# Kernel optimization log

Hardware: AMD Instinct MI355X
Metric: run time of the kernel (lower is better)

Reference implementation:

```python
import jax, jax.numpy as jnp
import numpy as np

KH, KW, PAD = 7, 7, 3  # 7x7 window, 'same' padding, stride 1


def setup_inputs() -> dict:
    key = jax.random.key(0)
    ks = jax.random.split(key, 7)
    b, c, h, w = 4, 256, 32, 32
    fc = 256
    rel_size = fc // 2
    ws = 1.0 / np.sqrt(c)
    rb = 1.0 / np.sqrt(rel_size)
    x = jax.random.normal(ks[0], (b, c, h, w), dtype=jnp.float32)
    Wq = jax.random.normal(ks[1], (c, fc), dtype=jnp.float32) * ws
    Wk = jax.random.normal(ks[2], (c, fc), dtype=jnp.float32) * ws
    Wv = jax.random.normal(ks[3], (c, fc), dtype=jnp.float32) * ws
    rel_x = jax.random.uniform(ks[4], (KW, rel_size), minval=-rb, maxval=rb, dtype=jnp.float32)
    rel_y = jax.random.uniform(ks[5], (KH, fc - rel_size), minval=-rb, maxval=rb, dtype=jnp.float32)
    bias = jax.random.uniform(ks[6], (fc,), minval=-1.0 / np.sqrt(fc), maxval=1.0 / np.sqrt(fc), dtype=jnp.float32)
    return {"x": x, "Wq": Wq, "Wk": Wk, "Wv": Wv, "rel_x": rel_x, "rel_y": rel_y, "bias": bias}


def _windows(t, kh, kw, pad):
    # t: (b, f, h, w) -> (b, f, kh*kw, h, w); stride-1 'same' window extraction
    b, f, h, w = t.shape
    tp = jnp.pad(t, ((0, 0), (0, 0), (pad, pad), (pad, pad)))
    return jnp.stack([tp[:, :, i:i + h, j:j + w] for i in range(kh) for j in range(kw)], axis=2)


def reference(x, Wq, Wk, Wv, rel_x, rel_y, bias):
    fc = Wq.shape[1]
    # per-pixel 1x1 projections (equivalent to projecting unfolded windows)
    q = jnp.einsum('bchw,cf->bfhw', x, Wq)  # center-pixel query
    k = jnp.einsum('bchw,cf->bfhw', x, Wk)
    v = jnp.einsum('bchw,cf->bfhw', x, Wv)
    kwin = _windows(k, KH, KW, PAD)  # (b, fc, K, h, w)
    vwin = _windows(v, KH, KW, PAD)
    # relative positional embedding: rel[ky, kx] = concat(rel_x[kx], rel_y[ky])
    rel = jnp.concatenate([
        jnp.broadcast_to(rel_x[None, :, :], (KH, KW, rel_x.shape[1])),
        jnp.broadcast_to(rel_y[:, None, :], (KH, KW, rel_y.shape[1])),
    ], axis=-1)  # (KH, KW, fc)
    rel = rel.reshape(KH * KW, fc).T[None, :, :, None, None]  # (1, fc, K, 1, 1)
    # per-channel score q * (k + rel), softmax over the window axis
    ab = q[:, :, None, :, :] * (kwin + rel)  # (b, fc, K, h, w)
    attn = jax.nn.softmax(ab, axis=2)
    out = (attn * vwin).sum(axis=2) + bias[None, :, None, None]
    return out
```

## Files before the change

### kernel.cpp

```cpp
#include <hip/hip_runtime.h>
#include <math.h>

#define C   256
#define FC  256
#define H   32
#define W   32
#define HW  1024
#define KH  7
#define KW  7
#define PAD 3
#define KK  49

typedef short s16x8 __attribute__((ext_vector_type(8)));
typedef float f32x4 __attribute__((ext_vector_type(4)));

__device__ __forceinline__ ushort f2bf(float f) {
    uint u = __float_as_uint(f);
    u += 0x7FFFu + ((u >> 16) & 1u);
    return (ushort)(u >> 16);
}
__device__ __forceinline__ float bf2f(ushort u) {
    return __uint_as_float(((uint)u) << 16);
}

__global__ __launch_bounds__(256) void prep_kernel(
    const float* __restrict__ x, const float* __restrict__ Wq,
    const float* __restrict__ Wk, const float* __restrict__ Wv,
    ushort* __restrict__ Xt, ushort* __restrict__ Wt)
{
    const int id = blockIdx.x;
    const float* src; ushort* dst; int sstride;
    if (id < 256) {
        int b = id >> 6, pxt = (id >> 2) & 15, ct = id & 3;
        src = x + ((size_t)(b * C + ct * 64)) * HW + pxt * 64;
        sstride = HW;
        dst = Xt + ((size_t)(b * HW + pxt * 64)) * C + ct * 64;
    } else {
        int wid = id - 256;
        int mat = wid >> 4, ft = (wid >> 2) & 3, ct = wid & 3;
        const float* Ws = (mat == 0) ? Wq : (mat == 1) ? Wk : Wv;
        src = Ws + ((size_t)(ct * 64)) * FC + ft * 64;
        sstride = FC;
        dst = Wt + ((size_t)(mat * FC + ft * 64)) * C + ct * 64;
    }
    const int t   = threadIdx.x;
    const int col = t & 63;
    const int rq  = t >> 6;
    ushort tmp[16];
    #pragma unroll
    for (int i = 0; i < 16; ++i)
        tmp[i] = f2bf(src[(size_t)(rq * 16 + i) * sstride + col]);
    #pragma unroll
    for (int i = 0; i < 4; ++i) {
        ushort4 u = make_ushort4(tmp[i*4], tmp[i*4+1], tmp[i*4+2], tmp[i*4+3]);
        *(ushort4*)&dst[(size_t)col * C + rq * 16 + i * 4] = u;
    }
}

__global__ __launch_bounds__(256) void qkv_mfma_kernel(
    const ushort* __restrict__ Xt, const ushort* __restrict__ Wt,
    ushort* __restrict__ qo, ushort* __restrict__ ko, ushort* __restrict__ vo)
{
    __shared__ ushort Xs[64][256];
    const int t   = threadIdx.x;
    const int pxt = blockIdx.x;
    const int fg  = blockIdx.y;
    const int b   = blockIdx.z;

    const ushort* Xtb = Xt + ((size_t)(b * HW + pxt * 64)) * C;
    #pragma unroll
    for (int i = 0; i < 8; ++i) {
        int idx = t + i * 256;
        int r = idx >> 5, c = idx & 31;
        *(s16x8*)&Xs[r][((c ^ (r & 7)) << 3)] =
            *(const s16x8*)&Xtb[(size_t)r * C + (c << 3)];
    }
    __syncthreads();

    const int wid = t >> 6, lane = t & 63;
    const int wf = wid >> 1, wp = wid & 1;
    const int lr = lane & 15;
    const int g  = lane >> 4;
    const int fbase = fg * 32 + wf * 16;
    const int pxb   = wp * 32;
    const int r7    = lr & 7;

    const ushort* a0p = Wt + ((size_t)(0 * FC + fbase + lr)) * C + g * 8;
    const ushort* a1p = Wt + ((size_t)(1 * FC + fbase + lr)) * C + g * 8;
    const ushort* a2p = Wt + ((size_t)(2 * FC + fbase + lr)) * C + g * 8;
    const ushort* xr0 = &Xs[pxb + lr][0];
    const ushort* xr1 = &Xs[pxb + 16 + lr][0];

    f32x4 acc00 = {0.f,0.f,0.f,0.f}, acc01 = {0.f,0.f,0.f,0.f};
    f32x4 acc10 = {0.f,0.f,0.f,0.f}, acc11 = {0.f,0.f,0.f,0.f};
    f32x4 acc20 = {0.f,0.f,0.f,0.f}, acc21 = {0.f,0.f,0.f,0.f};

    #pragma unroll
    for (int kk = 0; kk < 8; ++kk) {
        const int k0  = kk * 32;
        const int swo = ((kk * 4 + g) ^ r7) << 3;
        s16x8 a0 = *(const s16x8*)(a0p + k0);
        s16x8 a1 = *(const s16x8*)(a1p + k0);
        s16x8 a2 = *(const s16x8*)(a2p + k0);
        s16x8 b0 = *(const s16x8*)(xr0 + swo);
        s16x8 b1 = *(const s16x8*)(xr1 + swo);
        acc00 = __builtin_amdgcn_mfma_f32_16x16x32_bf16(a0, b0, acc00, 0, 0, 0);
        acc01 = __builtin_amdgcn_mfma_f32_16x16x32_bf16(a0, b1, acc01, 0, 0, 0);
        acc10 = __builtin_amdgcn_mfma_f32_16x16x32_bf16(a1, b0, acc10, 0, 0, 0);
        acc11 = __builtin_amdgcn_mfma_f32_16x16x32_bf16(a1, b1, acc11, 0, 0, 0);
        acc20 = __builtin_amdgcn_mfma_f32_16x16x32_bf16(a2, b0, acc20, 0, 0, 0);
        acc21 = __builtin_amdgcn_mfma_f32_16x16x32_bf16(a2, b1, acc21, 0, 0, 0);
    }

    const int fg4 = g * 4;
    const int px0 = pxt * 64 + pxb + lr;
    #pragma unroll
    for (int j = 0; j < 4; ++j) {
        size_t ro = ((size_t)(b * FC + fbase + fg4 + j)) * HW + px0;
        qo[ro]      = f2bf(acc00[j]);
        qo[ro + 16] = f2bf(acc01[j]);
        ko[ro]      = f2bf(acc10[j]);
        ko[ro + 16] = f2bf(acc11[j]);
        vo[ro]      = f2bf(acc20[j]);
        vo[ro + 16] = f2bf(acc21[j]);
    }
}

__global__ __launch_bounds__(256) void attn_kernel(
    const ushort* __restrict__ q, const ushort* __restrict__ k,
    const ushort* __restrict__ v,
    const float* __restrict__ rel_x, const float* __restrict__ rel_y,
    const float* __restrict__ bias, float* __restrict__ out)
{
    __shared__ float ks[22][22];
    __shared__ float vs[22][22];
    __shared__ float rel_s[KK];

    const int b   = blockIdx.z;
    const int f   = blockIdx.y;
    const int th0 = (blockIdx.x >> 1) * 16;
    const int tw0 = (blockIdx.x & 1) * 16;
    const int tid = threadIdx.x;
    const int tx  = tid & 15;
    const int ty  = tid >> 4;

    if (tid < KK) {
        int dy = tid / KW, dx = tid % KW;
        rel_s[tid] = (f < 128) ? rel_x[dx * 128 + f]
                               : rel_y[dy * 128 + (f - 128)];
    }

    const ushort* kb = k + ((size_t)b * FC + f) * HW;
    const ushort* vb = v + ((size_t)b * FC + f) * HW;
    for (int i = tid; i < 22 * 22; i += 256) {
        int r = i / 22, c2 = i % 22;
        int hh = th0 - PAD + r;
        int ww = tw0 - PAD + c2;
        bool in = (hh >= 0) & (hh < H) & (ww >= 0) & (ww < W);
        ks[r][c2] = in ? bf2f(kb[hh * W + ww]) : 0.f;
        vs[r][c2] = in ? bf2f(vb[hh * W + ww]) : 0.f;
    }
    __syncthreads();

    const int hh = th0 + ty, ww = tw0 + tx;
    const float qv = bf2f(q[((size_t)b * FC + f) * HW + hh * W + ww]);

    float tt[KK];
    float m = -INFINITY;
    #pragma unroll
    for (int ki = 0; ki < KK; ++ki) {
        int dy = ki / KW, dx = ki % KW;
        float s = qv * (ks[ty + dy][tx + dx] + rel_s[ki]);
        tt[ki] = s;
        m = fmaxf(m, s);
    }

    float sum = 0.f, acc = 0.f;
    #pragma unroll
    for (int ki = 0; ki < KK; ++ki) {
        int dy = ki / KW, dx = ki % KW;
        float e = __expf(tt[ki] - m);
        sum += e;
        acc = fmaf(e, vs[ty + dy][tx + dx], acc);
    }

    out[((size_t)b * FC + f) * HW + hh * W + ww] = acc / sum + bias[f];
}

extern "C" void kernel_launch(void* const* d_in, const int* in_sizes, int n_in,
                              void* d_out, int out_size, void* d_ws, size_t ws_size,
                              hipStream_t stream)
{
    const float* x     = (const float*)d_in[0];
    const float* Wq    = (const float*)d_in[1];
    const float* Wk    = (const float*)d_in[2];
    const float* Wv    = (const float*)d_in[3];
    const float* rel_x = (const float*)d_in[4];
    const float* rel_y = (const float*)d_in[5];
    const float* bias  = (const float*)d_in[6];
    float* out = (float*)d_out;

    ushort* Xt  = (ushort*)d_ws;
    ushort* Wtp = Xt + (size_t)4 * HW * C;
    ushort* q   = Wtp + (size_t)3 * FC * C;
    ushort* kk  = q + (size_t)4 * FC * HW;
    ushort* vv  = kk + (size_t)4 * FC * HW;

    prep_kernel<<<304, 256, 0, stream>>>(x, Wq, Wk, Wv, Xt, Wtp);
    qkv_mfma_kernel<<<dim3(16, 8, 4), 256, 0, stream>>>(Xt, Wtp, q, kk, vv);
    attn_kernel<<<dim3(4, FC, 4), 256, 0, stream>>>(q, kk, vv, rel_x, rel_y, bias, out);
}
```

Measured before the change: 37.12 us.

## Fuse bf16 conversion into QKV MFMA kernel, reading fp32 inputs directly

Removes the separate prep kernel that transposed and converted x and the weights to bf16 workspace buffers. The QKV MFMA kernel now loads fp32 x and W directly from global memory with strided scalar loads, converts in registers, and feeds the MFMAs. This eliminates one launch and a workspace write/read round trip, at the cost of less coalesced loads, redundant fp32 reads across blocks, and no LDS staging.

```diff
diff --git a/kernel.cpp b/kernel.cpp
--- a/kernel.cpp
+++ b/kernel.cpp
@@ -22,74 +22,35 @@
 __device__ __forceinline__ float bf2f(ushort u) {
     return __uint_as_float(((uint)u) << 16);
 }
-
-__global__ __launch_bounds__(256) void prep_kernel(
-    const float* __restrict__ x, const float* __restrict__ Wq,
-    const float* __restrict__ Wk, const float* __restrict__ Wv,
-    ushort* __restrict__ Xt, ushort* __restrict__ Wt)
-{
-    const int id = blockIdx.x;
-    const float* src; ushort* dst; int sstride;
-    if (id < 256) {
-        int b = id >> 6, pxt = (id >> 2) & 15, ct = id & 3;
-        src = x + ((size_t)(b * C + ct * 64)) * HW + pxt * 64;
-        sstride = HW;
-        dst = Xt + ((size_t)(b * HW + pxt * 64)) * C + ct * 64;
-    } else {
-        int wid = id - 256;
-        int mat = wid >> 4, ft = (wid >> 2) & 3, ct = wid & 3;
-        const float* Ws = (mat == 0) ? Wq : (mat == 1) ? Wk : Wv;
-        src = Ws + ((size_t)(ct * 64)) * FC + ft * 64;
-        sstride = FC;
-        dst = Wt + ((size_t)(mat * FC + ft * 64)) * C + ct * 64;
-    }
-    const int t   = threadIdx.x;
-    const int col = t & 63;
-    const int rq  = t >> 6;
-    ushort tmp[16];
+__device__ __forceinline__ s16x8 pack8(const float* v) {
+    s16x8 r;
     #pragma unroll
-    for (int i = 0; i < 16; ++i)
-        tmp[i] = f2bf(src[(size_t)(rq * 16 + i) * sstride + col]);
-    #pragma unroll
-    for (int i = 0; i < 4; ++i) {
-        ushort4 u = make_ushort4(tmp[i*4], tmp[i*4+1], tmp[i*4+2], tmp[i*4+3]);
-        *(ushort4*)&dst[(size_t)col * C + rq * 16 + i * 4] = u;
-    }
+    for (int j = 0; j < 8; ++j) r[j] = (short)f2bf(v[j]);
+    return r;
 }
 
-__global__ __launch_bounds__(256) void qkv_mfma_kernel(
-    const ushort* __restrict__ Xt, const ushort* __restrict__ Wt,
+__global__ __launch_bounds__(256) void qkv_direct_kernel(
+    const float* __restrict__ x,  const float* __restrict__ Wq,
+    const float* __restrict__ Wk, const float* __restrict__ Wv,
     ushort* __restrict__ qo, ushort* __restrict__ ko, ushort* __restrict__ vo)
 {
-    __shared__ ushort Xs[64][256];
     const int t   = threadIdx.x;
     const int pxt = blockIdx.x;
     const int fg  = blockIdx.y;
     const int b   = blockIdx.z;
-
-    const ushort* Xtb = Xt + ((size_t)(b * HW + pxt * 64)) * C;
-    #pragma unroll
-    for (int i = 0; i < 8; ++i) {
-        int idx = t + i * 256;
-        int r = idx >> 5, c = idx & 31;
-        *(s16x8*)&Xs[r][((c ^ (r & 7)) << 3)] =
-            *(const s16x8*)&Xtb[(size_t)r * C + (c << 3)];
-    }
-    __syncthreads();
 
     const int wid = t >> 6, lane = t & 63;
     const int wf = wid >> 1, wp = wid & 1;
     const int lr = lane & 15;
     const int g  = lane >> 4;
     const int fbase = fg * 32 + wf * 16;
-    const int pxb   = wp * 32;
-    const int r7    = lr & 7;
+    const int px0   = pxt * 64 + wp * 32 + lr;
 
-    const ushort* a0p = Wt + ((size_t)(0 * FC + fbase + lr)) * C + g * 8;
-    const ushort* a1p = Wt + ((size_t)(1 * FC + fbase + lr)) * C + g * 8;
-    const ushort* a2p = Wt + ((size_t)(2 * FC + fbase + lr)) * C + g * 8;
-    const ushort* xr0 = &Xs[pxb + lr][0];
-    const ushort* xr1 = &Xs[pxb + 16 + lr][0];
+    const float* wqp = Wq + (size_t)(g * 8) * FC + fbase + lr;
+    const float* wkp = Wk + (size_t)(g * 8) * FC + fbase + lr;
+    const float* wvp = Wv + (size_t)(g * 8) * FC + fbase + lr;
+    const float* xp0 = x + ((size_t)b * C + g * 8) * HW + px0;
+    const float* xp1 = xp0 + 16;
 
     f32x4 acc00 = {0.f,0.f,0.f,0.f}, acc01 = {0.f,0.f,0.f,0.f};
     f32x4 acc10 = {0.f,0.f,0.f,0.f}, acc11 = {0.f,0.f,0.f,0.f};
@@ -97,23 +58,27 @@
 
     #pragma unroll
     for (int kk = 0; kk < 8; ++kk) {
-        const int k0  = kk * 32;
-        const int swo = ((kk * 4 + g) ^ r7) << 3;
-        s16x8 a0 = *(const s16x8*)(a0p + k0);
-        s16x8 a1 = *(const s16x8*)(a1p + k0);
-        s16x8 a2 = *(const s16x8*)(a2p + k0);
-        s16x8 b0 = *(const s16x8*)(xr0 + swo);
-        s16x8 b1 = *(const s16x8*)(xr1 + swo);
-        acc00 = __builtin_amdgcn_mfma_f32_16x16x32_bf16(a0, b0, acc00, 0, 0, 0);
-        acc01 = __builtin_amdgcn_mfma_f32_16x16x32_bf16(a0, b1, acc01, 0, 0, 0);
-        acc10 = __builtin_amdgcn_mfma_f32_16x16x32_bf16(a1, b0, acc10, 0, 0, 0);
-        acc11 = __builtin_amdgcn_mfma_f32_16x16x32_bf16(a1, b1, acc11, 0, 0, 0);
-        acc20 = __builtin_amdgcn_mfma_f32_16x16x32_bf16(a2, b0, acc20, 0, 0, 0);
-        acc21 = __builtin_amdgcn_mfma_f32_16x16x32_bf16(a2, b1, acc21, 0, 0, 0);
+        const int co = kk * 32;
+        float aq[8], ak[8], av[8], b0[8], b1[8];
+        #pragma unroll
+        for (int j = 0; j < 8; ++j) {
+            aq[j] = wqp[(size_t)(co + j) * FC];
+            ak[j] = wkp[(size_t)(co + j) * FC];
+            av[j] = wvp[(size_t)(co + j) * FC];
+            b0[j] = xp0[(size_t)(co + j) * HW];
+            b1[j] = xp1[(size_t)(co + j) * HW];
+        }
+        s16x8 A0 = pack8(aq), A1 = pack8(ak), A2 = pack8(av);
+        s16x8 B0 = pack8(b0), B1 = pack8(b1);
+        acc00 = __builtin_amdgcn_mfma_f32_16x16x32_bf16(A0, B0, acc00, 0, 0, 0);
+        acc01 = __builtin_amdgcn_mfma_f32_16x16x32_bf16(A0, B1, acc01, 0, 0, 0);
+        acc10 = __builtin_amdgcn_mfma_f32_16x16x32_bf16(A1, B0, acc10, 0, 0, 0);
+        acc11 = __builtin_amdgcn_mfma_f32_16x16x32_bf16(A1, B1, acc11, 0, 0, 0);
+        acc20 = __builtin_amdgcn_mfma_f32_16x16x32_bf16(A2, B0, acc20, 0, 0, 0);
+        acc21 = __builtin_amdgcn_mfma_f32_16x16x32_bf16(A2, B1, acc21, 0, 0, 0);
     }
 
     const int fg4 = g * 4;
-    const int px0 = pxt * 64 + pxb + lr;
     #pragma unroll
     for (int j = 0; j < 4; ++j) {
         size_t ro = ((size_t)(b * FC + fbase + fg4 + j)) * HW + px0;
@@ -200,13 +165,10 @@
     const float* bias  = (const float*)d_in[6];
     float* out = (float*)d_out;
 
-    ushort* Xt  = (ushort*)d_ws;
-    ushort* Wtp = Xt + (size_t)4 * HW * C;
-    ushort* q   = Wtp + (size_t)3 * FC * C;
-    ushort* kk  = q + (size_t)4 * FC * HW;
-    ushort* vv  = kk + (size_t)4 * FC * HW;
+    ushort* q  = (ushort*)d_ws;
+    ushort* kk = q  + (size_t)4 * FC * HW;
+    ushort* vv = kk + (size_t)4 * FC * HW;
 
-    prep_kernel<<<304, 256, 0, stream>>>(x, Wq, Wk, Wv, Xt, Wtp);
-    qkv_mfma_kernel<<<dim3(16, 8, 4), 256, 0, stream>>>(Xt, Wtp, q, kk, vv);
+    qkv_direct_kernel<<<dim3(16, 8, 4), 256, 0, stream>>>(x, Wq, Wk, Wv, q, kk, vv);
     attn_kernel<<<dim3(4, FC, 4), 256, 0, stream>>>(q, kk, vv, rel_x, rel_y, bias, out);
 }
```

After: 32.29 us. 1.15x faster.
